# Optimization experiments

Measured on AMD Instinct MI355X. Metric: run time of the kernel, lower is better.

## Reference

```python
import jax, jax.numpy as jnp
import numpy as np

# ---- config (PointRCNN RPN, KITTI Car) ----
LOC_SCOPE = 3.0
LOC_BIN_SIZE = 0.5
NUM_HEAD_BIN = 12
PER_LOC_BIN = int(LOC_SCOPE / LOC_BIN_SIZE) * 2           # 12
REG_CH = PER_LOC_BIN * 4 + 1 + NUM_HEAD_BIN * 2 + 3       # 76
B, N = 4, 16384
RPN_PRE_NMS_TOP_N = 9000
RPN_POST_NMS_TOP_N = 512
NMS_THRESH = 0.8
PRE = RPN_PRE_NMS_TOP_N // B    # 2250 per image
POST = RPN_POST_NMS_TOP_N // B  # 128 per image
TWO_PI = 2.0 * np.pi


def _gather1(a, idx):
    # a: (M, K), idx: (M,) -> (M,)
    return jnp.take_along_axis(a, idx[:, None], axis=1)[:, 0]


def decode_bbox_target(xyz, reg, anchor):
    """xyz: (M,3) roi centers, reg: (M,76) -> (M,7) [x,y,z,h,w,l,ry]."""
    pb = PER_LOC_BIN
    dt = reg.dtype
    x_bin = jnp.argmax(reg[:, 0:pb], axis=1)
    z_bin = jnp.argmax(reg[:, pb:2 * pb], axis=1)
    pos_x = x_bin.astype(dt) * LOC_BIN_SIZE + LOC_BIN_SIZE / 2 - LOC_SCOPE
    pos_z = z_bin.astype(dt) * LOC_BIN_SIZE + LOC_BIN_SIZE / 2 - LOC_SCOPE
    # fine xz residuals (LOC_XZ_FINE=True)
    pos_x = pos_x + _gather1(reg[:, 2 * pb:3 * pb], x_bin) * LOC_BIN_SIZE
    pos_z = pos_z + _gather1(reg[:, 3 * pb:4 * pb], z_bin) * LOC_BIN_SIZE
    so = 4 * pb
    pos_y = xyz[:, 1] + reg[:, so]                  # get_y_by_bin=False
    rb = so + 1
    ry_bin = jnp.argmax(reg[:, rb:rb + NUM_HEAD_BIN], axis=1)
    ry_res_norm = _gather1(reg[:, rb + NUM_HEAD_BIN:rb + 2 * NUM_HEAD_BIN], ry_bin)
    apc = TWO_PI / NUM_HEAD_BIN                     # get_ry_fine=False
    ry = (ry_bin.astype(dt) * apc + ry_res_norm * (apc / 2)) % TWO_PI
    ry = jnp.where(ry > np.pi, ry - TWO_PI, ry)
    hwl = reg[:, -3:] * anchor + anchor             # (M,3) h,w,l
    return jnp.concatenate([
        (pos_x + xyz[:, 0])[:, None], pos_y[:, None], (pos_z + xyz[:, 2])[:, None],
        hwl, ry[:, None]], axis=1)


def _greedy_nms(iou):
    """iou: (K,K) for boxes sorted by score desc -> keep mask (K,)."""
    K = iou.shape[0]
    ar = jnp.arange(K)
    def body(i, sup):
        keep_i = jnp.logical_not(sup[i])
        return sup | (keep_i & (iou[i] > NMS_THRESH) & (ar > i))
    sup = jax.lax.fori_loop(0, K, body, jnp.zeros((K,), jnp.bool_))
    return jnp.logical_not(sup)


def _forward(rpn_scores, rpn_reg, xyz, anchor_size):
    boxes = decode_bbox_target(xyz.reshape(-1, 3), rpn_reg.reshape(-1, REG_CH), anchor_size)
    boxes = boxes.at[:, 1].add(boxes[:, 3] * 0.5)   # y += h/2
    boxes = boxes.reshape(B, N, 7)
    # per-image sort by score desc, take pre-NMS top-n (score_based_proposal)
    order = jnp.argsort(-rpn_scores, axis=1)[:, :PRE]           # (B, PRE)
    sc = jnp.take_along_axis(rpn_scores, order, axis=1)         # (B, PRE)
    pr = jnp.take_along_axis(boxes, order[:, :, None], axis=1)  # (B, PRE, 7)
    # BEV boxes (nms_normal: axis-aligned IoU of [x1,z1,x2,z2])
    cb = jax.lax.stop_gradient(pr)
    x1 = cb[..., 0] - cb[..., 5] * 0.5
    x2 = cb[..., 0] + cb[..., 5] * 0.5
    z1 = cb[..., 2] - cb[..., 4] * 0.5
    z2 = cb[..., 2] + cb[..., 4] * 0.5
    area = (x2 - x1) * (z2 - z1)                                 # (B, PRE)
    iw = jnp.maximum(jnp.minimum(x2[:, :, None], x2[:, None, :]) -
                     jnp.maximum(x1[:, :, None], x1[:, None, :]), 0.0)
    ih = jnp.maximum(jnp.minimum(z2[:, :, None], z2[:, None, :]) -
                     jnp.maximum(z1[:, :, None], z1[:, None, :]), 0.0)
    inter = iw * ih
    iou = inter / (area[:, :, None] + area[:, None, :] - inter)  # (B, PRE, PRE)
    kept = jax.vmap(_greedy_nms)(iou)                            # (B, PRE) bool
    keep_idx = jax.vmap(lambda m: jnp.nonzero(m, size=POST, fill_value=-1)[0])(kept)
    valid = keep_idx >= 0
    ki = jnp.maximum(keep_idx, 0)
    ret_bbox3d = jnp.where(valid[:, :, None],
                           jnp.take_along_axis(pr, ki[:, :, None], axis=1), 0.0)
    ret_scores = jnp.where(valid, jnp.take_along_axis(sc, ki, axis=1), 0.0)
    return ret_bbox3d, ret_scores                                # (B,POST,7), (B,POST)


def setup_inputs() -> dict:
    key = jax.random.key(0)
    k1, k2, k3 = jax.random.split(key, 3)
    return {
        "rpn_scores": jax.random.normal(k1, (B, N), jnp.float32),
        "rpn_reg": jax.random.normal(k2, (B, N, REG_CH), jnp.float32),
        "xyz": jax.random.normal(k3, (B, N, 3), jnp.float32) * 20.0,  # KITTI-scale coords
        "anchor_size": jnp.array([1.52, 1.63, 3.88], jnp.float32),    # MEAN_SIZE (h,w,l)
    }


def reference(rpn_scores, rpn_reg, xyz, anchor_size):
    return _forward(rpn_scores, rpn_reg, xyz, anchor_size)
```

## Files before the change

### kernel.cpp

```cpp
#include <hip/hip_runtime.h>
#include <stdint.h>

#define BN 4
#define NPTS 16384
#define REGC 76
#define PRE 2250
#define PRE_PAD 2304
#define POST 128
#define NBINS 4096
#define NB2 8192
#define SORTN 4096
#define ECAP 4096
#define NMS_T 0.8f
#define TI 18
#define NTRI 171
#define SZB (BN * PRE_PAD)
#define DECB 9

__device__ __forceinline__ uint32_t flip_f32(float f) {
  uint32_t u = __float_as_uint(f);
  return (u & 0x80000000u) ? ~u : (u | 0x80000000u);
}
__device__ __forceinline__ float unflip_f32(uint32_t k) {
  uint32_t u = (k & 0x80000000u) ? (k & 0x7FFFFFFFu) : ~k;
  return __uint_as_float(u);
}

__device__ __forceinline__ uint32_t fine_key(uint32_t flp, int bt) {
  const int d = (int)(flp >> 20) - bt;
  return (d >= 31) ? 8191u : (((uint32_t)d << 8) | ((flp >> 12) & 0xFFu));
}

__global__ __launch_bounds__(1024) void k_histrank(
    const float* __restrict__ scores, uint32_t* __restrict__ srt,
    float* __restrict__ ws_score, int* __restrict__ edge_cnt) {
  __shared__ uint32_t h2[NB2];
  __shared__ uint32_t o2[NB2];
  __shared__ unsigned long long skey[SORTN];
  __shared__ uint32_t wsum[16];
  __shared__ int s_bt, s_cnt;
  const int img = blockIdx.x, tid = threadIdx.x;
  const int wave = tid >> 6, lane = tid & 63;
  const float* sc = scores + img * NPTS;

  for (int i = tid; i < NBINS; i += 1024) h2[i] = 0u;
  if (tid == 0) edge_cnt[img] = 0;
  __syncthreads();

  uint32_t k0[16];
#pragma unroll
  for (int r = 0; r < 16; ++r) {
    k0[r] = flip_f32(sc[tid + r * 1024]);
    atomicAdd(&h2[k0[r] >> 20], 1u);
  }
  __syncthreads();

  const uint32_t c0 = h2[4 * tid + 0], c1 = h2[4 * tid + 1];
  const uint32_t c2 = h2[4 * tid + 2], c3 = h2[4 * tid + 3];
  uint32_t s3 = c3, s2 = c2 + s3, s1 = c1 + s2, s0 = c0 + s1;
  const uint32_t tot = s0;
  uint32_t run = tot;
#pragma unroll
  for (int off = 1; off < 64; off <<= 1) {
    uint32_t v = __shfl_down(run, off);
    if (lane + off < 64) run += v;
  }
  if (lane == 0) wsum[wave] = run;
  __syncthreads();
  uint32_t tail = 0;
  for (int w = wave + 1; w < 16; ++w) tail += wsum[w];
  const uint32_t after = run - tot + tail;
  const uint32_t S0 = s0 + after, S1 = s1 + after, S2 = s2 + after,
                 S3 = s3 + after;
  const uint32_t P = PRE;
  if (S0 >= P && S1 < P) { s_bt = 4 * tid + 0; s_cnt = (int)S0; }
  if (S1 >= P && S2 < P) { s_bt = 4 * tid + 1; s_cnt = (int)S1; }
  if (S2 >= P && S3 < P) { s_bt = 4 * tid + 2; s_cnt = (int)S2; }
  if (S3 >= P && after < P) { s_bt = 4 * tid + 3; s_cnt = (int)S3; }
  __syncthreads();
  const int bt = s_bt;

  for (int i = tid; i < NB2; i += 1024) h2[i] = 0u;
  __syncthreads();
#pragma unroll
  for (int r = 0; r < 16; ++r) {
    if ((int)(k0[r] >> 20) >= bt) atomicAdd(&h2[fine_key(k0[r], bt)], 1u);
  }
  __syncthreads();

  uint32_t cc[8], ss[8];
#pragma unroll
  for (int j = 0; j < 8; ++j) cc[j] = h2[8 * tid + j];
  uint32_t acc2 = 0;
#pragma unroll
  for (int j = 7; j >= 0; --j) { acc2 += cc[j]; ss[j] = acc2; }
  const uint32_t tot2 = acc2;
  uint32_t run2 = tot2;
#pragma unroll
  for (int off = 1; off < 64; off <<= 1) {
    uint32_t v = __shfl_down(run2, off);
    if (lane + off < 64) run2 += v;
  }
  if (lane == 0) wsum[wave] = run2;
  __syncthreads();
  uint32_t tail2 = 0;
  for (int w = wave + 1; w < 16; ++w) tail2 += wsum[w];
  const uint32_t after2 = run2 - tot2 + tail2;
#pragma unroll
  for (int j = 0; j < 8; ++j) {
    o2[8 * tid + j] = cc[j];
    h2[8 * tid + j] = ((j < 7) ? ss[j + 1] : 0u) + after2;
  }
  __syncthreads();

#pragma unroll
  for (int r = 0; r < 16; ++r) {
    if ((int)(k0[r] >> 20) >= bt) {
      uint32_t pos = atomicAdd(&h2[fine_key(k0[r], bt)], 1u);
      if (pos < SORTN)
        skey[pos] =
            ((unsigned long long)(~k0[r]) << 32) | (uint32_t)(tid + r * 1024);
    }
  }
  __syncthreads();

  const int cnt = s_cnt < SORTN ? s_cnt : SORTN;
  for (int i = tid; i < cnt; i += 1024) {
    const unsigned long long myk = skey[i];
    const uint32_t flp = ~(uint32_t)(myk >> 32);
    const uint32_t key2 = fine_key(flp, bt);
    const int base2 = (int)h2[key2] - (int)o2[key2];
    int end = (int)h2[key2];
    end = end < SORTN ? end : SORTN;
    int rank = base2;
    for (int q = base2; q < end; ++q) rank += (int)(skey[q] < myk);
    if (rank >= PRE) continue;
    srt[img * PRE_PAD + rank] = (uint32_t)myk;
    ws_score[img * PRE_PAD + rank] = unflip_f32(~(uint32_t)(myk >> 32));
  }
}

__global__ __launch_bounds__(256) void k_dec(
    const uint32_t* __restrict__ srt, const float* __restrict__ reg,
    const float* __restrict__ xyz, const float* __restrict__ anchor,
    float* __restrict__ ws_pr, float* __restrict__ bev) {
  const int img = blockIdx.x / DECB;
  const int r = (blockIdx.x % DECB) * 256 + threadIdx.x;
  if (r >= PRE) return;
  const int idx = (int)srt[img * PRE_PAD + r];

  const float* rr = reg + (size_t)(img * NPTS + idx) * REGC;
  float v[REGC];
  const float4* r4 = reinterpret_cast<const float4*>(rr);
#pragma unroll
  for (int qq = 0; qq < REGC / 4; ++qq) {
    float4 f = r4[qq];
    v[4 * qq + 0] = f.x; v[4 * qq + 1] = f.y;
    v[4 * qq + 2] = f.z; v[4 * qq + 3] = f.w;
  }

  int xb = 0; float xm = v[0];
#pragma unroll
  for (int c = 1; c < 12; ++c) if (v[c] > xm) { xm = v[c]; xb = c; }
  int zb = 0; float zm = v[12];
#pragma unroll
  for (int c = 1; c < 12; ++c) if (v[12 + c] > zm) { zm = v[12 + c]; zb = c; }
  float xres = v[24];
#pragma unroll
  for (int c = 1; c < 12; ++c) if (xb == c) xres = v[24 + c];
  float zres = v[36];
#pragma unroll
  for (int c = 1; c < 12; ++c) if (zb == c) zres = v[36 + c];

  float posx = xb * 0.5f + 0.25f - 3.0f + xres * 0.5f;
  float posz = zb * 0.5f + 0.25f - 3.0f + zres * 0.5f;

  const float* xp = xyz + (size_t)(img * NPTS + idx) * 3;
  float X = posx + xp[0];
  float Y = xp[1] + v[48];
  float Z = posz + xp[2];

  int ryb = 0; float rym = v[49];
#pragma unroll
  for (int c = 1; c < 12; ++c) if (v[49 + c] > rym) { rym = v[49 + c]; ryb = c; }
  float ryres = v[61];
#pragma unroll
  for (int c = 1; c < 12; ++c) if (ryb == c) ryres = v[61 + c];

  const float APC = 0.5235987755982988f;
  const float APC2 = 0.2617993877991494f;
  const float TWO_PI_F = 6.283185307179586f;
  const float PI_F = 3.141592653589793f;
  float ry = ryb * APC + ryres * APC2;
  ry = fmodf(ry, TWO_PI_F);
  if (ry < 0.0f) ry += TWO_PI_F;
  if (ry > PI_F) ry -= TWO_PI_F;

  float ah = anchor[0], aw = anchor[1], al = anchor[2];
  float H = v[73] * ah + ah;
  float W = v[74] * aw + aw;
  float L = v[75] * al + al;
  Y += H * 0.5f;

  float* pr = ws_pr + (size_t)(img * PRE_PAD + r) * 7;
  pr[0] = X; pr[1] = Y; pr[2] = Z; pr[3] = H; pr[4] = W; pr[5] = L; pr[6] = ry;

  int o = img * PRE_PAD + r;
  float x1 = X - L * 0.5f, x2 = X + L * 0.5f;
  float z1 = Z - W * 0.5f, z2 = Z + W * 0.5f;
  bev[o] = x1;
  bev[SZB + o] = x2;
  bev[2 * SZB + o] = z1;
  bev[3 * SZB + o] = z2;
  bev[4 * SZB + o] = (x2 - x1) * (z2 - z1);
}

__global__ __launch_bounds__(256) void k_pairs(
    const float* __restrict__ bev, uint32_t* __restrict__ edges,
    int* __restrict__ edge_cnt) {
  int bx = blockIdx.x;
  int img = bx / NTRI;
  int t = bx - img * NTRI;
  int ti = 0, acc = 0;
#pragma unroll
  for (int row = 0; row < TI; ++row) {
    int c = TI - row;
    if (t < acc + c) { ti = row; break; }
    acc += c;
  }
  int tj = ti + (t - acc);

  __shared__ float rx1[128], rx2[128], rz1[128], rz2[128], ra[128];
  __shared__ float cx1[128], cx2[128], cz1[128], cz2[128], ca[128];
  int tid = threadIdx.x;
  if (tid < 128) {
    int o = img * PRE_PAD + ti * 128 + tid;
    rx1[tid] = bev[o];           rx2[tid] = bev[SZB + o];
    rz1[tid] = bev[2 * SZB + o]; rz2[tid] = bev[3 * SZB + o];
    ra[tid] = bev[4 * SZB + o];
  } else {
    int q = tid - 128;
    int o = img * PRE_PAD + tj * 128 + q;
    cx1[q] = bev[o];             cx2[q] = bev[SZB + o];
    cz1[q] = bev[2 * SZB + o];   cz2[q] = bev[3 * SZB + o];
    ca[q] = bev[4 * SZB + o];
  }
  __syncthreads();

  const int b = tid & 127;
  const int a0 = tid >> 7;
  const float bx1 = cx1[b], bx2 = cx2[b], bz1 = cz1[b], bz2 = cz2[b],
              bar = ca[b];
  const int j = tj * 128 + b;
  for (int a = a0; a < 128; a += 2) {
    int i = ti * 128 + a;
    if (i < j && j < PRE) {
      float iw = fminf(rx2[a], bx2) - fmaxf(rx1[a], bx1);
      iw = fmaxf(iw, 0.0f);
      float ih = fminf(rz2[a], bz2) - fmaxf(rz1[a], bz1);
      ih = fmaxf(ih, 0.0f);
      float inter = iw * ih;
      float iou = inter / (ra[a] + bar - inter);
      if (iou > NMS_T) {
        int e = atomicAdd(&edge_cnt[img], 1);
        if (e < ECAP) edges[img * ECAP + e] = ((uint32_t)i << 16) | (uint32_t)j;
      }
    }
  }
}

__global__ __launch_bounds__(1024) void k_resolve(
    const uint32_t* __restrict__ edges, const int* __restrict__ edge_cnt,
    const float* __restrict__ ws_pr, const float* __restrict__ ws_score,
    float* __restrict__ out) {
  __shared__ uint32_t sup[PRE];
  __shared__ uint32_t earr[ECAP];
  __shared__ uint32_t wtot[16];
  const int img = blockIdx.x, tid = threadIdx.x;
  const int wave = tid >> 6, lane = tid & 63;

  for (int i = tid; i < PRE; i += 1024) sup[i] = 0u;
  int E = edge_cnt[img];
  E = E < 0 ? 0 : (E > ECAP ? ECAP : E);
  int P2 = 1;
  while (P2 < E) P2 <<= 1;
  for (int e = tid; e < P2; e += 1024)
    earr[e] = (e < E) ? edges[img * ECAP + e] : 0xFFFFFFFFu;
  __syncthreads();

  for (int k = 2; k <= P2; k <<= 1)
    for (int j = k >> 1; j > 0; j >>= 1) {
      for (int t = tid; t < (P2 >> 1); t += 1024) {
        int ii = ((t & ~(j - 1)) << 1) | (t & (j - 1));
        int l = ii | j;
        uint32_t a = earr[ii], b = earr[l];
        if ((a > b) == ((ii & k) == 0)) { earr[ii] = b; earr[l] = a; }
      }
      __syncthreads();
    }

  if (tid == 0) {
    int lastsi = -1;
    uint32_t keep_si = 0u;
    for (int e = 0; e < E; ++e) {
      uint32_t u = earr[e];
      int si = (int)(u >> 16), sj = (int)(u & 0xFFFFu);
      if (si != lastsi) { lastsi = si; keep_si = !sup[si]; }
      if (keep_si) sup[sj] = 1u;
    }
  }
  __syncthreads();

  const int q0 = 4 * tid;
  uint32_t f0 = (q0 + 0 < PRE && !sup[q0 + 0]) ? 1u : 0u;
  uint32_t f1 = (q0 + 1 < PRE && !sup[q0 + 1]) ? 1u : 0u;
  uint32_t f2 = (q0 + 2 < PRE && !sup[q0 + 2]) ? 1u : 0u;
  uint32_t f3 = (q0 + 3 < PRE && !sup[q0 + 3]) ? 1u : 0u;
  uint32_t p0 = f0, p1 = p0 + f1, p2 = p1 + f2, p3 = p2 + f3;
  const uint32_t tot = p3;
  uint32_t run = tot;
#pragma unroll
  for (int off = 1; off < 64; off <<= 1) {
    uint32_t v = __shfl_up(run, off);
    if (lane >= off) run += v;
  }
  if (lane == 63) wtot[wave] = run;
  __syncthreads();
  uint32_t wbase = 0, total = 0;
  for (int w = 0; w < 16; ++w) {
    uint32_t t = wtot[w];
    if (w < wave) wbase += t;
    total += t;
  }
  const uint32_t before = wbase + run - tot;

  float* ob = out + (size_t)img * POST * 7;
  float* os = out + (size_t)(BN * POST * 7) + img * POST;
  uint32_t fc[4] = {f0, f1, f2, f3};
  uint32_t pc[4] = {p0, p1, p2, p3};
#pragma unroll
  for (int c = 0; c < 4; ++c) {
    if (fc[c]) {
      int rk = (int)(before + pc[c]) - 1;
      if (rk < POST) {
        const float* p = ws_pr + (size_t)(img * PRE_PAD + (q0 + c)) * 7;
#pragma unroll
        for (int cc = 0; cc < 7; ++cc) ob[rk * 7 + cc] = p[cc];
        os[rk] = ws_score[img * PRE_PAD + (q0 + c)];
      }
    }
  }
  for (int rk = (int)total + tid; rk < POST; rk += 1024) {
#pragma unroll
    for (int cc = 0; cc < 7; ++cc) ob[rk * 7 + cc] = 0.0f;
    os[rk] = 0.0f;
  }
}

extern "C" void kernel_launch(void* const* d_in, const int* in_sizes, int n_in,
                              void* d_out, int out_size, void* d_ws, size_t ws_size,
                              hipStream_t stream) {
  const float* scores = (const float*)d_in[0];
  const float* reg = (const float*)d_in[1];
  const float* xyz = (const float*)d_in[2];
  const float* anchor = (const float*)d_in[3];
  float* out = (float*)d_out;
  char* ws = (char*)d_ws;

  uint32_t* edges = (uint32_t*)(ws + 0);
  float* ws_score = (float*)(ws + 65536);
  float* ws_pr = (float*)(ws + 102400);
  float* bev = (float*)(ws + 360448);
  int* edge_cnt = (int*)(ws + 544768);
  uint32_t* srt = (uint32_t*)(ws + 544800);

  k_histrank<<<BN, 1024, 0, stream>>>(scores, srt, ws_score, edge_cnt);
  k_dec<<<BN * DECB, 256, 0, stream>>>(srt, reg, xyz, anchor, ws_pr, bev);
  k_pairs<<<BN * NTRI, 256, 0, stream>>>(bev, edges, edge_cnt);
  k_resolve<<<BN, 1024, 0, stream>>>(edges, edge_cnt, ws_pr, ws_score, out);
}
```

Baseline: 106.6 us.

## Fuse all stages into one cooperative kernel with grid syncs and split histogram

```diff
diff --git a/kernel.cpp b/kernel.cpp
--- a/kernel.cpp
+++ b/kernel.cpp
@@ -1,5 +1,8 @@
 #include <hip/hip_runtime.h>
+#include <hip/hip_cooperative_groups.h>
 #include <stdint.h>
+
+namespace cg = cooperative_groups;
 
 #define BN 4
 #define NPTS 16384
@@ -15,7 +18,8 @@
 #define TI 18
 #define NTRI 171
 #define SZB (BN * PRE_PAD)
-#define DECB 9
+#define GRID 192
+#define HPARTS 8
 
 __device__ __forceinline__ uint32_t flip_f32(float f) {
   uint32_t u = __float_as_uint(f);
@@ -31,329 +35,366 @@
   return (d >= 31) ? 8191u : (((uint32_t)d << 8) | ((flp >> 12) & 0xFFu));
 }
 
-__global__ __launch_bounds__(1024) void k_histrank(
-    const float* __restrict__ scores, uint32_t* __restrict__ srt,
-    float* __restrict__ ws_score, int* __restrict__ edge_cnt) {
-  __shared__ uint32_t h2[NB2];
-  __shared__ uint32_t o2[NB2];
-  __shared__ unsigned long long skey[SORTN];
-  __shared__ uint32_t wsum[16];
-  __shared__ int s_bt, s_cnt;
-  const int img = blockIdx.x, tid = threadIdx.x;
+struct P1 {
+  uint32_t h2[NB2];
+  uint32_t o2[NB2];
+  unsigned long long skey[SORTN];
+  uint32_t wsum[16];
+  int s_bt, s_cnt;
+};
+struct P3 {
+  float rx1[128], rx2[128], rz1[128], rz2[128], ra[128];
+  float cx1[128], cx2[128], cz1[128], cz2[128], ca[128];
+};
+struct P4 {
+  uint32_t sup[PRE];
+  uint32_t earr[ECAP];
+  uint32_t wtot[16];
+};
+union SMem { P1 p1; P3 p3; P4 p4; };
+
+__global__ __launch_bounds__(1024) void k_all(
+    const float* __restrict__ scores, const float* __restrict__ reg,
+    const float* __restrict__ xyz, const float* __restrict__ anchor,
+    float* __restrict__ out, float* __restrict__ ws_score,
+    float* __restrict__ ws_pr, float* __restrict__ bev,
+    int* __restrict__ edge_cnt, uint32_t* __restrict__ edges,
+    uint32_t* __restrict__ srt, uint32_t* __restrict__ phist) {
+  cg::grid_group grid = cg::this_grid();
+  __shared__ SMem sm;
+  const int blk = blockIdx.x, tid = threadIdx.x;
   const int wave = tid >> 6, lane = tid & 63;
-  const float* sc = scores + img * NPTS;
-
-  for (int i = tid; i < NBINS; i += 1024) h2[i] = 0u;
-  if (tid == 0) edge_cnt[img] = 0;
-  __syncthreads();
-
-  uint32_t k0[16];
-#pragma unroll
-  for (int r = 0; r < 16; ++r) {
-    k0[r] = flip_f32(sc[tid + r * 1024]);
-    atomicAdd(&h2[k0[r] >> 20], 1u);
+
+  if (blk < BN * HPARTS) {
+    const int img = blk >> 3, part = blk & (HPARTS - 1);
+    uint32_t* h = sm.p1.h2;
+    for (int i = tid; i < NBINS; i += 1024) h[i] = 0u;
+    __syncthreads();
+    const float* sc = scores + img * NPTS + part * (NPTS / HPARTS);
+#pragma unroll
+    for (int k = 0; k < NPTS / HPARTS / 1024; ++k)
+      atomicAdd(&h[flip_f32(sc[k * 1024 + tid]) >> 20], 1u);
+    __syncthreads();
+    uint32_t* dst = phist + (size_t)(img * HPARTS + part) * NBINS;
+    for (int i = tid; i < NBINS; i += 1024) dst[i] = h[i];
   }
-  __syncthreads();
-
-  const uint32_t c0 = h2[4 * tid + 0], c1 = h2[4 * tid + 1];
-  const uint32_t c2 = h2[4 * tid + 2], c3 = h2[4 * tid + 3];
-  uint32_t s3 = c3, s2 = c2 + s3, s1 = c1 + s2, s0 = c0 + s1;
-  const uint32_t tot = s0;
-  uint32_t run = tot;
-#pragma unroll
-  for (int off = 1; off < 64; off <<= 1) {
-    uint32_t v = __shfl_down(run, off);
-    if (lane + off < 64) run += v;
+  if (blk == BN * HPARTS && tid < BN) edge_cnt[tid] = 0;
+  grid.sync();
+
+  if (blk < BN) {
+    const int img = blk;
+    uint32_t* h2 = sm.p1.h2;
+    uint32_t* o2 = sm.p1.o2;
+    unsigned long long* skey = sm.p1.skey;
+    const uint32_t* ph = phist + (size_t)img * HPARTS * NBINS;
+    for (int i = tid; i < NBINS; i += 1024) {
+      uint32_t s = 0;
+#pragma unroll
+      for (int p = 0; p < HPARTS; ++p) s += ph[p * NBINS + i];
+      h2[i] = s;
+    }
+    __syncthreads();
+
+    const uint32_t c0 = h2[4 * tid + 0], c1 = h2[4 * tid + 1];
+    const uint32_t c2 = h2[4 * tid + 2], c3 = h2[4 * tid + 3];
+    uint32_t s3 = c3, s2 = c2 + s3, s1 = c1 + s2, s0 = c0 + s1;
+    const uint32_t tot = s0;
+    uint32_t run = tot;
+#pragma unroll
+    for (int off = 1; off < 64; off <<= 1) {
+      uint32_t v = __shfl_down(run, off);
+      if (lane + off < 64) run += v;
+    }
+    if (lane == 0) sm.p1.wsum[wave] = run;
+    __syncthreads();
+    uint32_t tail = 0;
+    for (int w = wave + 1; w < 16; ++w) tail += sm.p1.wsum[w];
+    const uint32_t after = run - tot + tail;
+    const uint32_t S0 = s0 + after, S1 = s1 + after, S2 = s2 + after,
+                   S3 = s3 + after;
+    const uint32_t P = PRE;
+    if (S0 >= P && S1 < P) { sm.p1.s_bt = 4 * tid + 0; sm.p1.s_cnt = (int)S0; }
+    if (S1 >= P && S2 < P) { sm.p1.s_bt = 4 * tid + 1; sm.p1.s_cnt = (int)S1; }
+    if (S2 >= P && S3 < P) { sm.p1.s_bt = 4 * tid + 2; sm.p1.s_cnt = (int)S2; }
+    if (S3 >= P && after < P) { sm.p1.s_bt = 4 * tid + 3; sm.p1.s_cnt = (int)S3; }
+    __syncthreads();
+    const int bt = sm.p1.s_bt;
+
+    const float* sc = scores + img * NPTS;
+    uint32_t k0[16];
+#pragma unroll
+    for (int r = 0; r < 16; ++r) k0[r] = flip_f32(sc[tid + r * 1024]);
+
+    for (int i = tid; i < NB2; i += 1024) h2[i] = 0u;
+    __syncthreads();
+#pragma unroll
+    for (int r = 0; r < 16; ++r) {
+      if ((int)(k0[r] >> 20) >= bt) atomicAdd(&h2[fine_key(k0[r], bt)], 1u);
+    }
+    __syncthreads();
+
+    uint32_t cc[8], ss[8];
+#pragma unroll
+    for (int j = 0; j < 8; ++j) cc[j] = h2[8 * tid + j];
+    uint32_t acc2 = 0;
+#pragma unroll
+    for (int j = 7; j >= 0; --j) { acc2 += cc[j]; ss[j] = acc2; }
+    const uint32_t tot2 = acc2;
+    uint32_t run2 = tot2;
+#pragma unroll
+    for (int off = 1; off < 64; off <<= 1) {
+      uint32_t v = __shfl_down(run2, off);
+      if (lane + off < 64) run2 += v;
+    }
+    if (lane == 0) sm.p1.wsum[wave] = run2;
+    __syncthreads();
+    uint32_t tail2 = 0;
+    for (int w = wave + 1; w < 16; ++w) tail2 += sm.p1.wsum[w];
+    const uint32_t after2 = run2 - tot2 + tail2;
+#pragma unroll
+    for (int j = 0; j < 8; ++j) {
+      o2[8 * tid + j] = cc[j];
+      h2[8 * tid + j] = ((j < 7) ? ss[j + 1] : 0u) + after2;
+    }
+    __syncthreads();
+
+#pragma unroll
+    for (int r = 0; r < 16; ++r) {
+      if ((int)(k0[r] >> 20) >= bt) {
+        uint32_t pos = atomicAdd(&h2[fine_key(k0[r], bt)], 1u);
+        if (pos < SORTN)
+          skey[pos] = ((unsigned long long)(~k0[r]) << 32) |
+                      (uint32_t)(tid + r * 1024);
+      }
+    }
+    __syncthreads();
+
+    const int cnt = sm.p1.s_cnt < SORTN ? sm.p1.s_cnt : SORTN;
+    for (int i = tid; i < cnt; i += 1024) {
+      const unsigned long long myk = skey[i];
+      const uint32_t flp = ~(uint32_t)(myk >> 32);
+      const uint32_t key2 = fine_key(flp, bt);
+      const int base2 = (int)h2[key2] - (int)o2[key2];
+      int end = (int)h2[key2];
+      end = end < SORTN ? end : SORTN;
+      int rank = base2;
+      for (int q = base2; q < end; ++q) rank += (int)(skey[q] < myk);
+      if (rank >= PRE) continue;
+      srt[img * PRE_PAD + rank] = (uint32_t)myk;
+      ws_score[img * PRE_PAD + rank] = unflip_f32(~(uint32_t)(myk >> 32));
+    }
   }
-  if (lane == 0) wsum[wave] = run;
-  __syncthreads();
-  uint32_t tail = 0;
-  for (int w = wave + 1; w < 16; ++w) tail += wsum[w];
-  const uint32_t after = run - tot + tail;
-  const uint32_t S0 = s0 + after, S1 = s1 + after, S2 = s2 + after,
-                 S3 = s3 + after;
-  const uint32_t P = PRE;
-  if (S0 >= P && S1 < P) { s_bt = 4 * tid + 0; s_cnt = (int)S0; }
-  if (S1 >= P && S2 < P) { s_bt = 4 * tid + 1; s_cnt = (int)S1; }
-  if (S2 >= P && S3 < P) { s_bt = 4 * tid + 2; s_cnt = (int)S2; }
-  if (S3 >= P && after < P) { s_bt = 4 * tid + 3; s_cnt = (int)S3; }
-  __syncthreads();
-  const int bt = s_bt;
-
-  for (int i = tid; i < NB2; i += 1024) h2[i] = 0u;
-  __syncthreads();
-#pragma unroll
-  for (int r = 0; r < 16; ++r) {
-    if ((int)(k0[r] >> 20) >= bt) atomicAdd(&h2[fine_key(k0[r], bt)], 1u);
+  grid.sync();
+
+  {
+    const int job = blk * 1024 + tid;
+    if (job < BN * PRE) {
+      const int img = job / PRE;
+      const int r = job - img * PRE;
+      const int idx = (int)srt[img * PRE_PAD + r];
+
+      const float* rr = reg + (size_t)(img * NPTS + idx) * REGC;
+      float v[REGC];
+      const float4* r4 = reinterpret_cast<const float4*>(rr);
+#pragma unroll
+      for (int qq = 0; qq < REGC / 4; ++qq) {
+        float4 f = r4[qq];
+        v[4 * qq + 0] = f.x; v[4 * qq + 1] = f.y;
+        v[4 * qq + 2] = f.z; v[4 * qq + 3] = f.w;
+      }
+
+      int xb = 0; float xm = v[0];
+#pragma unroll
+      for (int c = 1; c < 12; ++c) if (v[c] > xm) { xm = v[c]; xb = c; }
+      int zb = 0; float zm = v[12];
+#pragma unroll
+      for (int c = 1; c < 12; ++c) if (v[12 + c] > zm) { zm = v[12 + c]; zb = c; }
+      float xres = v[24];
+#pragma unroll
+      for (int c = 1; c < 12; ++c) if (xb == c) xres = v[24 + c];
+      float zres = v[36];
+#pragma unroll
+      for (int c = 1; c < 12; ++c) if (zb == c) zres = v[36 + c];
+
+      float posx = xb * 0.5f + 0.25f - 3.0f + xres * 0.5f;
+      float posz = zb * 0.5f + 0.25f - 3.0f + zres * 0.5f;
+
+      const float* xp = xyz + (size_t)(img * NPTS + idx) * 3;
+      float X = posx + xp[0];
+      float Y = xp[1] + v[48];
+      float Z = posz + xp[2];
+
+      int ryb = 0; float rym = v[49];
+#pragma unroll
+      for (int c = 1; c < 12; ++c)
+        if (v[49 + c] > rym) { rym = v[49 + c]; ryb = c; }
+      float ryres = v[61];
+#pragma unroll
+      for (int c = 1; c < 12; ++c) if (ryb == c) ryres = v[61 + c];
+
+      const float APC = 0.5235987755982988f;
+      const float APC2 = 0.2617993877991494f;
+      const float TWO_PI_F = 6.283185307179586f;
+      const float PI_F = 3.141592653589793f;
+      float ry = ryb * APC + ryres * APC2;
+      ry = fmodf(ry, TWO_PI_F);
+      if (ry < 0.0f) ry += TWO_PI_F;
+      if (ry > PI_F) ry -= TWO_PI_F;
+
+      float ah = anchor[0], aw = anchor[1], al = anchor[2];
+      float H = v[73] * ah + ah;
+      float W = v[74] * aw + aw;
+      float L = v[75] * al + al;
+      Y += H * 0.5f;
+
+      float* pr = ws_pr + (size_t)(img * PRE_PAD + r) * 7;
+      pr[0] = X; pr[1] = Y; pr[2] = Z; pr[3] = H; pr[4] = W; pr[5] = L;
+      pr[6] = ry;
+
+      int o = img * PRE_PAD + r;
+      float x1 = X - L * 0.5f, x2 = X + L * 0.5f;
+      float z1 = Z - W * 0.5f, z2 = Z + W * 0.5f;
+      bev[o] = x1;
+      bev[SZB + o] = x2;
+      bev[2 * SZB + o] = z1;
+      bev[3 * SZB + o] = z2;
+      bev[4 * SZB + o] = (x2 - x1) * (z2 - z1);
+    }
   }
-  __syncthreads();
-
-  uint32_t cc[8], ss[8];
-#pragma unroll
-  for (int j = 0; j < 8; ++j) cc[j] = h2[8 * tid + j];
-  uint32_t acc2 = 0;
-#pragma unroll
-  for (int j = 7; j >= 0; --j) { acc2 += cc[j]; ss[j] = acc2; }
-  const uint32_t tot2 = acc2;
-  uint32_t run2 = tot2;
-#pragma unroll
-  for (int off = 1; off < 64; off <<= 1) {
-    uint32_t v = __shfl_down(run2, off);
-    if (lane + off < 64) run2 += v;
+  grid.sync();
+
+  for (int t5 = blk; t5 < BN * NTRI; t5 += GRID) {
+    const int img = t5 / NTRI;
+    const int t = t5 - img * NTRI;
+    int ti = 0, acc = 0;
+#pragma unroll
+    for (int row = 0; row < TI; ++row) {
+      int c = TI - row;
+      if (t < acc + c) { ti = row; break; }
+      acc += c;
+    }
+    const int tj = ti + (t - acc);
+
+    __syncthreads();
+    if (tid < 128) {
+      int o = img * PRE_PAD + ti * 128 + tid;
+      sm.p3.rx1[tid] = bev[o];           sm.p3.rx2[tid] = bev[SZB + o];
+      sm.p3.rz1[tid] = bev[2 * SZB + o]; sm.p3.rz2[tid] = bev[3 * SZB + o];
+      sm.p3.ra[tid] = bev[4 * SZB + o];
+    } else if (tid < 256) {
+      int q = tid - 128;
+      int o = img * PRE_PAD + tj * 128 + q;
+      sm.p3.cx1[q] = bev[o];             sm.p3.cx2[q] = bev[SZB + o];
+      sm.p3.cz1[q] = bev[2 * SZB + o];   sm.p3.cz2[q] = bev[3 * SZB + o];
+      sm.p3.ca[q] = bev[4 * SZB + o];
+    }
+    __syncthreads();
+
+    const int b = tid & 127;
+    const int a0 = tid >> 7;
+    const float bx1 = sm.p3.cx1[b], bx2 = sm.p3.cx2[b], bz1 = sm.p3.cz1[b],
+                bz2 = sm.p3.cz2[b], bar = sm.p3.ca[b];
+    const int j = tj * 128 + b;
+    for (int a = a0; a < 128; a += 8) {
+      int i = ti * 128 + a;
+      if (i < j && j < PRE) {
+        float iw = fminf(sm.p3.rx2[a], bx2) - fmaxf(sm.p3.rx1[a], bx1);
+        iw = fmaxf(iw, 0.0f);
+        float ih = fminf(sm.p3.rz2[a], bz2) - fmaxf(sm.p3.rz1[a], bz1);
+        ih = fmaxf(ih, 0.0f);
+        float inter = iw * ih;
+        float iou = inter / (sm.p3.ra[a] + bar - inter);
+        if (iou > NMS_T) {
+          int e = atomicAdd(&edge_cnt[img], 1);
+          if (e < ECAP)
+            edges[img * ECAP + e] = ((uint32_t)i << 16) | (uint32_t)j;
+        }
+      }
+    }
   }
-  if (lane == 0) wsum[wave] = run2;
-  __syncthreads();
-  uint32_t tail2 = 0;
-  for (int w = wave + 1; w < 16; ++w) tail2 += wsum[w];
-  const uint32_t after2 = run2 - tot2 + tail2;
-#pragma unroll
-  for (int j = 0; j < 8; ++j) {
-    o2[8 * tid + j] = cc[j];
-    h2[8 * tid + j] = ((j < 7) ? ss[j + 1] : 0u) + after2;
-  }
-  __syncthreads();
-
-#pragma unroll
-  for (int r = 0; r < 16; ++r) {
-    if ((int)(k0[r] >> 20) >= bt) {
-      uint32_t pos = atomicAdd(&h2[fine_key(k0[r], bt)], 1u);
-      if (pos < SORTN)
-        skey[pos] =
-            ((unsigned long long)(~k0[r]) << 32) | (uint32_t)(tid + r * 1024);
-    }
-  }
-  __syncthreads();
-
-  const int cnt = s_cnt < SORTN ? s_cnt : SORTN;
-  for (int i = tid; i < cnt; i += 1024) {
-    const unsigned long long myk = skey[i];
-    const uint32_t flp = ~(uint32_t)(myk >> 32);
-    const uint32_t key2 = fine_key(flp, bt);
-    const int base2 = (int)h2[key2] - (int)o2[key2];
-    int end = (int)h2[key2];
-    end = end < SORTN ? end : SORTN;
-    int rank = base2;
-    for (int q = base2; q < end; ++q) rank += (int)(skey[q] < myk);
-    if (rank >= PRE) continue;
-    srt[img * PRE_PAD + rank] = (uint32_t)myk;
-    ws_score[img * PRE_PAD + rank] = unflip_f32(~(uint32_t)(myk >> 32));
-  }
-}
-
-__global__ __launch_bounds__(256) void k_dec(
-    const uint32_t* __restrict__ srt, const float* __restrict__ reg,
-    const float* __restrict__ xyz, const float* __restrict__ anchor,
-    float* __restrict__ ws_pr, float* __restrict__ bev) {
-  const int img = blockIdx.x / DECB;
-  const int r = (blockIdx.x % DECB) * 256 + threadIdx.x;
-  if (r >= PRE) return;
-  const int idx = (int)srt[img * PRE_PAD + r];
-
-  const float* rr = reg + (size_t)(img * NPTS + idx) * REGC;
-  float v[REGC];
-  const float4* r4 = reinterpret_cast<const float4*>(rr);
-#pragma unroll
-  for (int qq = 0; qq < REGC / 4; ++qq) {
-    float4 f = r4[qq];
-    v[4 * qq + 0] = f.x; v[4 * qq + 1] = f.y;
-    v[4 * qq + 2] = f.z; v[4 * qq + 3] = f.w;
-  }
-
-  int xb = 0; float xm = v[0];
-#pragma unroll
-  for (int c = 1; c < 12; ++c) if (v[c] > xm) { xm = v[c]; xb = c; }
-  int zb = 0; float zm = v[12];
-#pragma unroll
-  for (int c = 1; c < 12; ++c) if (v[12 + c] > zm) { zm = v[12 + c]; zb = c; }
-  float xres = v[24];
-#pragma unroll
-  for (int c = 1; c < 12; ++c) if (xb == c) xres = v[24 + c];
-  float zres = v[36];
-#pragma unroll
-  for (int c = 1; c < 12; ++c) if (zb == c) zres = v[36 + c];
-
-  float posx = xb * 0.5f + 0.25f - 3.0f + xres * 0.5f;
-  float posz = zb * 0.5f + 0.25f - 3.0f + zres * 0.5f;
-
-  const float* xp = xyz + (size_t)(img * NPTS + idx) * 3;
-  float X = posx + xp[0];
-  float Y = xp[1] + v[48];
-  float Z = posz + xp[2];
-
-  int ryb = 0; float rym = v[49];
-#pragma unroll
-  for (int c = 1; c < 12; ++c) if (v[49 + c] > rym) { rym = v[49 + c]; ryb = c; }
-  float ryres = v[61];
-#pragma unroll
-  for (int c = 1; c < 12; ++c) if (ryb == c) ryres = v[61 + c];
-
-  const float APC = 0.5235987755982988f;
-  const float APC2 = 0.2617993877991494f;
-  const float TWO_PI_F = 6.283185307179586f;
-  const float PI_F = 3.141592653589793f;
-  float ry = ryb * APC + ryres * APC2;
-  ry = fmodf(ry, TWO_PI_F);
-  if (ry < 0.0f) ry += TWO_PI_F;
-  if (ry > PI_F) ry -= TWO_PI_F;
-
-  float ah = anchor[0], aw = anchor[1], al = anchor[2];
-  float H = v[73] * ah + ah;
-  float W = v[74] * aw + aw;
-  float L = v[75] * al + al;
-  Y += H * 0.5f;
-
-  float* pr = ws_pr + (size_t)(img * PRE_PAD + r) * 7;
-  pr[0] = X; pr[1] = Y; pr[2] = Z; pr[3] = H; pr[4] = W; pr[5] = L; pr[6] = ry;
-
-  int o = img * PRE_PAD + r;
-  float x1 = X - L * 0.5f, x2 = X + L * 0.5f;
-  float z1 = Z - W * 0.5f, z2 = Z + W * 0.5f;
-  bev[o] = x1;
-  bev[SZB + o] = x2;
-  bev[2 * SZB + o] = z1;
-  bev[3 * SZB + o] = z2;
-  bev[4 * SZB + o] = (x2 - x1) * (z2 - z1);
-}
-
-__global__ __launch_bounds__(256) void k_pairs(
-    const float* __restrict__ bev, uint32_t* __restrict__ edges,
-    int* __restrict__ edge_cnt) {
-  int bx = blockIdx.x;
-  int img = bx / NTRI;
-  int t = bx - img * NTRI;
-  int ti = 0, acc = 0;
-#pragma unroll
-  for (int row = 0; row < TI; ++row) {
-    int c = TI - row;
-    if (t < acc + c) { ti = row; break; }
-    acc += c;
-  }
-  int tj = ti + (t - acc);
-
-  __shared__ float rx1[128], rx2[128], rz1[128], rz2[128], ra[128];
-  __shared__ float cx1[128], cx2[128], cz1[128], cz2[128], ca[128];
-  int tid = threadIdx.x;
-  if (tid < 128) {
-    int o = img * PRE_PAD + ti * 128 + tid;
-    rx1[tid] = bev[o];           rx2[tid] = bev[SZB + o];
-    rz1[tid] = bev[2 * SZB + o]; rz2[tid] = bev[3 * SZB + o];
-    ra[tid] = bev[4 * SZB + o];
-  } else {
-    int q = tid - 128;
-    int o = img * PRE_PAD + tj * 128 + q;
-    cx1[q] = bev[o];             cx2[q] = bev[SZB + o];
-    cz1[q] = bev[2 * SZB + o];   cz2[q] = bev[3 * SZB + o];
-    ca[q] = bev[4 * SZB + o];
-  }
-  __syncthreads();
-
-  const int b = tid & 127;
-  const int a0 = tid >> 7;
-  const float bx1 = cx1[b], bx2 = cx2[b], bz1 = cz1[b], bz2 = cz2[b],
-              bar = ca[b];
-  const int j = tj * 128 + b;
-  for (int a = a0; a < 128; a += 2) {
-    int i = ti * 128 + a;
-    if (i < j && j < PRE) {
-      float iw = fminf(rx2[a], bx2) - fmaxf(rx1[a], bx1);
-      iw = fmaxf(iw, 0.0f);
-      float ih = fminf(rz2[a], bz2) - fmaxf(rz1[a], bz1);
-      ih = fmaxf(ih, 0.0f);
-      float inter = iw * ih;
-      float iou = inter / (ra[a] + bar - inter);
-      if (iou > NMS_T) {
-        int e = atomicAdd(&edge_cnt[img], 1);
-        if (e < ECAP) edges[img * ECAP + e] = ((uint32_t)i << 16) | (uint32_t)j;
-      }
-    }
-  }
-}
-
-__global__ __launch_bounds__(1024) void k_resolve(
-    const uint32_t* __restrict__ edges, const int* __restrict__ edge_cnt,
-    const float* __restrict__ ws_pr, const float* __restrict__ ws_score,
-    float* __restrict__ out) {
-  __shared__ uint32_t sup[PRE];
-  __shared__ uint32_t earr[ECAP];
-  __shared__ uint32_t wtot[16];
-  const int img = blockIdx.x, tid = threadIdx.x;
-  const int wave = tid >> 6, lane = tid & 63;
-
-  for (int i = tid; i < PRE; i += 1024) sup[i] = 0u;
-  int E = edge_cnt[img];
-  E = E < 0 ? 0 : (E > ECAP ? ECAP : E);
-  int P2 = 1;
-  while (P2 < E) P2 <<= 1;
-  for (int e = tid; e < P2; e += 1024)
-    earr[e] = (e < E) ? edges[img * ECAP + e] : 0xFFFFFFFFu;
-  __syncthreads();
-
-  for (int k = 2; k <= P2; k <<= 1)
-    for (int j = k >> 1; j > 0; j >>= 1) {
-      for (int t = tid; t < (P2 >> 1); t += 1024) {
-        int ii = ((t & ~(j - 1)) << 1) | (t & (j - 1));
-        int l = ii | j;
-        uint32_t a = earr[ii], b = earr[l];
-        if ((a > b) == ((ii & k) == 0)) { earr[ii] = b; earr[l] = a; }
-      }
-      __syncthreads();
-    }
-
-  if (tid == 0) {
-    int lastsi = -1;
-    uint32_t keep_si = 0u;
-    for (int e = 0; e < E; ++e) {
-      uint32_t u = earr[e];
-      int si = (int)(u >> 16), sj = (int)(u & 0xFFFFu);
-      if (si != lastsi) { lastsi = si; keep_si = !sup[si]; }
-      if (keep_si) sup[sj] = 1u;
-    }
-  }
-  __syncthreads();
-
-  const int q0 = 4 * tid;
-  uint32_t f0 = (q0 + 0 < PRE && !sup[q0 + 0]) ? 1u : 0u;
-  uint32_t f1 = (q0 + 1 < PRE && !sup[q0 + 1]) ? 1u : 0u;
-  uint32_t f2 = (q0 + 2 < PRE && !sup[q0 + 2]) ? 1u : 0u;
-  uint32_t f3 = (q0 + 3 < PRE && !sup[q0 + 3]) ? 1u : 0u;
-  uint32_t p0 = f0, p1 = p0 + f1, p2 = p1 + f2, p3 = p2 + f3;
-  const uint32_t tot = p3;
-  uint32_t run = tot;
-#pragma unroll
-  for (int off = 1; off < 64; off <<= 1) {
-    uint32_t v = __shfl_up(run, off);
-    if (lane >= off) run += v;
-  }
-  if (lane == 63) wtot[wave] = run;
-  __syncthreads();
-  uint32_t wbase = 0, total = 0;
-  for (int w = 0; w < 16; ++w) {
-    uint32_t t = wtot[w];
-    if (w < wave) wbase += t;
-    total += t;
-  }
-  const uint32_t before = wbase + run - tot;
-
-  float* ob = out + (size_t)img * POST * 7;
-  float* os = out + (size_t)(BN * POST * 7) + img * POST;
-  uint32_t fc[4] = {f0, f1, f2, f3};
-  uint32_t pc[4] = {p0, p1, p2, p3};
-#pragma unroll
-  for (int c = 0; c < 4; ++c) {
-    if (fc[c]) {
-      int rk = (int)(before + pc[c]) - 1;
-      if (rk < POST) {
-        const float* p = ws_pr + (size_t)(img * PRE_PAD + (q0 + c)) * 7;
-#pragma unroll
-        for (int cc = 0; cc < 7; ++cc) ob[rk * 7 + cc] = p[cc];
-        os[rk] = ws_score[img * PRE_PAD + (q0 + c)];
-      }
-    }
-  }
-  for (int rk = (int)total + tid; rk < POST; rk += 1024) {
-#pragma unroll
-    for (int cc = 0; cc < 7; ++cc) ob[rk * 7 + cc] = 0.0f;
-    os[rk] = 0.0f;
+  grid.sync();
+
+  if (blk < BN) {
+    const int img = blk;
+    uint32_t* sup = sm.p4.sup;
+    uint32_t* earr = sm.p4.earr;
+
+    for (int i = tid; i < PRE; i += 1024) sup[i] = 0u;
+    int E = edge_cnt[img];
+    E = E < 0 ? 0 : (E > ECAP ? ECAP : E);
+    int P2 = 1;
+    while (P2 < E) P2 <<= 1;
+    for (int e = tid; e < P2; e += 1024)
+      earr[e] = (e < E) ? edges[img * ECAP + e] : 0xFFFFFFFFu;
+    __syncthreads();
+
+    for (int k = 2; k <= P2; k <<= 1)
+      for (int j = k >> 1; j > 0; j >>= 1) {
+        for (int t = tid; t < (P2 >> 1); t += 1024) {
+          int ii = ((t & ~(j - 1)) << 1) | (t & (j - 1));
+          int l = ii | j;
+          uint32_t a = earr[ii], b = earr[l];
+          if ((a > b) == ((ii & k) == 0)) { earr[ii] = b; earr[l] = a; }
+        }
+        __syncthreads();
+      }
+
+    if (tid == 0) {
+      int lastsi = -1;
+      uint32_t keep_si = 0u;
+      for (int e = 0; e < E; ++e) {
+        uint32_t u = earr[e];
+        int si = (int)(u >> 16), sj = (int)(u & 0xFFFFu);
+        if (si != lastsi) { lastsi = si; keep_si = !sup[si]; }
+        if (keep_si) sup[sj] = 1u;
+      }
+    }
+    __syncthreads();
+
+    const int q0 = 4 * tid;
+    uint32_t f0 = (q0 + 0 < PRE && !sup[q0 + 0]) ? 1u : 0u;
+    uint32_t f1 = (q0 + 1 < PRE && !sup[q0 + 1]) ? 1u : 0u;
+    uint32_t f2 = (q0 + 2 < PRE && !sup[q0 + 2]) ? 1u : 0u;
+    uint32_t f3 = (q0 + 3 < PRE && !sup[q0 + 3]) ? 1u : 0u;
+    uint32_t p0 = f0, p1 = p0 + f1, p2 = p1 + f2, p3 = p2 + f3;
+    const uint32_t tot = p3;
+    uint32_t run = tot;
+#pragma unroll
+    for (int off = 1; off < 64; off <<= 1) {
+      uint32_t v = __shfl_up(run, off);
+      if (lane >= off) run += v;
+    }
+    if (lane == 63) sm.p4.wtot[wave] = run;
+    __syncthreads();
+    uint32_t wbase = 0, total = 0;
+    for (int w = 0; w < 16; ++w) {
+      uint32_t t = sm.p4.wtot[w];
+      if (w < wave) wbase += t;
+      total += t;
+    }
+    const uint32_t before = wbase + run - tot;
+
+    float* ob = out + (size_t)img * POST * 7;
+    float* os = out + (size_t)(BN * POST * 7) + img * POST;
+    uint32_t fc[4] = {f0, f1, f2, f3};
+    uint32_t pc[4] = {p0, p1, p2, p3};
+#pragma unroll
+    for (int c = 0; c < 4; ++c) {
+      if (fc[c]) {
+        int rk = (int)(before + pc[c]) - 1;
+        if (rk < POST) {
+          const float* p = ws_pr + (size_t)(img * PRE_PAD + (q0 + c)) * 7;
+#pragma unroll
+          for (int cc = 0; cc < 7; ++cc) ob[rk * 7 + cc] = p[cc];
+          os[rk] = ws_score[img * PRE_PAD + (q0 + c)];
+        }
+      }
+    }
+    for (int rk = (int)total + tid; rk < POST; rk += 1024) {
+#pragma unroll
+      for (int cc = 0; cc < 7; ++cc) ob[rk * 7 + cc] = 0.0f;
+      os[rk] = 0.0f;
+    }
   }
 }
 
@@ -373,9 +414,12 @@
   float* bev = (float*)(ws + 360448);
   int* edge_cnt = (int*)(ws + 544768);
   uint32_t* srt = (uint32_t*)(ws + 544800);
-
-  k_histrank<<<BN, 1024, 0, stream>>>(scores, srt, ws_score, edge_cnt);
-  k_dec<<<BN * DECB, 256, 0, stream>>>(srt, reg, xyz, anchor, ws_pr, bev);
-  k_pairs<<<BN * NTRI, 256, 0, stream>>>(bev, edges, edge_cnt);
-  k_resolve<<<BN, 1024, 0, stream>>>(edges, edge_cnt, ws_pr, ws_score, out);
+  uint32_t* phist = (uint32_t*)(ws + 581664);
+
+  void* args[] = {(void*)&scores, (void*)&reg,      (void*)&xyz,
+                  (void*)&anchor, (void*)&out,      (void*)&ws_score,
+                  (void*)&ws_pr,  (void*)&bev,      (void*)&edge_cnt,
+                  (void*)&edges,  (void*)&srt,      (void*)&phist};
+  hipLaunchCooperativeKernel((const void*)k_all, dim3(GRID), dim3(1024), args,
+                             0, stream);
 }
```

Measured after the change: 211.3 us. +98.2%, slower.

## Split coarse score histogram across multiple blocks per image

Applied to the files above, without the earlier changes.

```diff
diff --git a/kernel.cpp b/kernel.cpp
--- a/kernel.cpp
+++ b/kernel.cpp
@@ -16,6 +16,7 @@
 #define NTRI 171
 #define SZB (BN * PRE_PAD)
 #define DECB 9
+#define HPARTS 8
 
 __device__ __forceinline__ uint32_t flip_f32(float f) {
   uint32_t u = __float_as_uint(f);
@@ -31,9 +32,27 @@
   return (d >= 31) ? 8191u : (((uint32_t)d << 8) | ((flp >> 12) & 0xFFu));
 }
 
-__global__ __launch_bounds__(1024) void k_histrank(
-    const float* __restrict__ scores, uint32_t* __restrict__ srt,
-    float* __restrict__ ws_score, int* __restrict__ edge_cnt) {
+__global__ __launch_bounds__(1024) void k_phist(
+    const float* __restrict__ scores, uint32_t* __restrict__ phist,
+    int* __restrict__ edge_cnt) {
+  __shared__ uint32_t h[NBINS];
+  const int blk = blockIdx.x, tid = threadIdx.x;
+  const int img = blk >> 3, part = blk & (HPARTS - 1);
+  for (int i = tid; i < NBINS; i += 1024) h[i] = 0u;
+  if (blk == 0 && tid < BN) edge_cnt[tid] = 0;
+  __syncthreads();
+  const float* sc = scores + img * NPTS + part * (NPTS / HPARTS);
+#pragma unroll
+  for (int k = 0; k < NPTS / HPARTS / 1024; ++k)
+    atomicAdd(&h[flip_f32(sc[k * 1024 + tid]) >> 20], 1u);
+  __syncthreads();
+  uint32_t* dst = phist + (size_t)(img * HPARTS + part) * NBINS;
+  for (int i = tid; i < NBINS; i += 1024) dst[i] = h[i];
+}
+
+__global__ __launch_bounds__(1024) void k_rank(
+    const float* __restrict__ scores, const uint32_t* __restrict__ phist,
+    uint32_t* __restrict__ srt, float* __restrict__ ws_score) {
   __shared__ uint32_t h2[NB2];
   __shared__ uint32_t o2[NB2];
   __shared__ unsigned long long skey[SORTN];
@@ -41,17 +60,13 @@
   __shared__ int s_bt, s_cnt;
   const int img = blockIdx.x, tid = threadIdx.x;
   const int wave = tid >> 6, lane = tid & 63;
-  const float* sc = scores + img * NPTS;
-
-  for (int i = tid; i < NBINS; i += 1024) h2[i] = 0u;
-  if (tid == 0) edge_cnt[img] = 0;
-  __syncthreads();
-
-  uint32_t k0[16];
-#pragma unroll
-  for (int r = 0; r < 16; ++r) {
-    k0[r] = flip_f32(sc[tid + r * 1024]);
-    atomicAdd(&h2[k0[r] >> 20], 1u);
+
+  const uint32_t* ph = phist + (size_t)img * HPARTS * NBINS;
+  for (int i = tid; i < NBINS; i += 1024) {
+    uint32_t s = 0;
+#pragma unroll
+    for (int p = 0; p < HPARTS; ++p) s += ph[p * NBINS + i];
+    h2[i] = s;
   }
   __syncthreads();
 
@@ -80,6 +95,11 @@
   __syncthreads();
   const int bt = s_bt;
 
+  const float* sc = scores + img * NPTS;
+  uint32_t k0[16];
+#pragma unroll
+  for (int r = 0; r < 16; ++r) k0[r] = flip_f32(sc[tid + r * 1024]);
+
   for (int i = tid; i < NB2; i += 1024) h2[i] = 0u;
   __syncthreads();
 #pragma unroll
@@ -118,8 +138,8 @@
     if ((int)(k0[r] >> 20) >= bt) {
       uint32_t pos = atomicAdd(&h2[fine_key(k0[r], bt)], 1u);
       if (pos < SORTN)
-        skey[pos] =
-            ((unsigned long long)(~k0[r]) << 32) | (uint32_t)(tid + r * 1024);
+        skey[pos] = ((unsigned long long)(~k0[r]) << 32) |
+                    (uint32_t)(tid + r * 1024);
     }
   }
   __syncthreads();
@@ -373,8 +393,10 @@
   float* bev = (float*)(ws + 360448);
   int* edge_cnt = (int*)(ws + 544768);
   uint32_t* srt = (uint32_t*)(ws + 544800);
-
-  k_histrank<<<BN, 1024, 0, stream>>>(scores, srt, ws_score, edge_cnt);
+  uint32_t* phist = (uint32_t*)(ws + 581664);
+
+  k_phist<<<BN * HPARTS, 1024, 0, stream>>>(scores, phist, edge_cnt);
+  k_rank<<<BN, 1024, 0, stream>>>(scores, phist, srt, ws_score);
   k_dec<<<BN * DECB, 256, 0, stream>>>(srt, reg, xyz, anchor, ws_pr, bev);
   k_pairs<<<BN * NTRI, 256, 0, stream>>>(bev, edges, edge_cnt);
   k_resolve<<<BN, 1024, 0, stream>>>(edges, edge_cnt, ws_pr, ws_score, out);
```

New measurement: 107.7 us. Within noise of the previous version (+1.0%).
